# Optimization experiments

Measured on AMD Instinct MI355X. Metric: run time of the kernel, lower is better.

## Reference

```python
import jax, jax.numpy as jnp
import numpy as np

B, NO, NM, NV, E = 16, 512, 128, 64, 256
H, DK, MS, FF = 16, 16, 8, 512
TRANS_MAX = 100.0


def _ln(x):
    m = x.mean(-1, keepdims=True)
    v = ((x - m) ** 2).mean(-1, keepdims=True)
    return (x - m) * jax.lax.rsqrt(v + 1e-5)


def _inv_norm(x):
    # 1 - minmax-normalize over the whole per-batch matrix
    mn = x.min(axis=(1, 2), keepdims=True)
    mx = x.max(axis=(1, 2), keepdims=True)
    return 1.0 - (x - mn) / (mx - mn)


def _adjacency(proc_time, trans_time, MVpair_trans, mask_dyn, mask_ma):
    # masked copy of proc_time
    A_proc = jnp.where(mask_dyn, proc_time, 0.0)
    # keep only the per-row minimum nonzero entry (min_ProcTime_elements)
    nz = jnp.where(A_proc == 0.0, jnp.inf, A_proc)
    mn = nz.min(axis=2, keepdims=True)
    keep = (A_proc == mn) & (A_proc != 0.0)
    A_proc = A_proc * keep.astype(proc_time.dtype)
    A_proc_norm = (A_proc > 0.0).astype(proc_time.dtype)
    # machine-machine masks
    mask2 = mask_ma[:, None, :] & mask_ma[:, :, None]  # [B, nm, nm]
    A_procing = (~mask2).astype(proc_time.dtype)
    A_off = _inv_norm(MVpair_trans)
    tt = jnp.where(mask2, trans_time, TRANS_MAX + 1.0)
    A_on = _inv_norm(tt)
    return A_proc_norm, A_procing, A_off, A_on


def _block(row, col, cost, Wq, Wk, Wv, Wo, mW1, mb1, mW2, mb2, fW1, fb1, fW2, fb2):
    # MatNet-style mixed-score multi-head attention encoding block
    Bb, R, _ = row.shape
    C = col.shape[1]
    q = (row @ Wq).reshape(Bb, R, H, DK).transpose(0, 2, 1, 3)  # bhrd
    k = (col @ Wk).reshape(Bb, C, H, DK).transpose(0, 2, 1, 3)  # bhcd
    v = (col @ Wv).reshape(Bb, C, H, DK).transpose(0, 2, 1, 3)
    dot = jnp.einsum('bhrd,bhcd->bhrc', q, k) / jnp.sqrt(jnp.asarray(DK, row.dtype))
    two = jnp.stack([dot, jnp.broadcast_to(cost[:, None], dot.shape)], axis=-1)  # [B,H,R,C,2]
    hmix = jax.nn.relu(jnp.einsum('bhrct,hts->bhrcs', two, mW1) + mb1[None, :, None, None, :])
    score = jnp.einsum('bhrcs,hso->bhrco', hmix, mW2)[..., 0] + mb2[:, 0][None, :, None, None]
    attn = jax.nn.softmax(score, axis=-1)
    ctx = jnp.einsum('bhrc,bhcd->bhrd', attn, v).transpose(0, 2, 1, 3).reshape(Bb, R, H * DK)
    out1 = _ln(row + ctx @ Wo)
    ffn = jax.nn.relu(out1 @ fW1 + fb1) @ fW2 + fb2
    return _ln(out1 + ffn)


def setup_inputs() -> dict:
    key = jax.random.key(0)
    ks = jax.random.split(key, 24)

    def nrm(i, shape, s=0.05):
        return jax.random.normal(ks[i], shape, jnp.float32) * s

    return {
        'ope_emb': nrm(0, (B, NO, E), 1.0),
        'ma_emb': nrm(1, (B, NM, E), 1.0),
        'veh_emb': nrm(2, (B, NV, E), 1.0),
        'proc_time': jax.random.uniform(ks[3], (B, NO, NM), jnp.float32) * 20.0,
        'offload_trans_time': jax.random.uniform(ks[4], (B, NO, NV), jnp.float32) * TRANS_MAX,
        'trans_time': jax.random.uniform(ks[5], (B, NM, NM), jnp.float32) * TRANS_MAX,
        'MVpair_trans': jax.random.uniform(ks[6], (B, NV, NM), jnp.float32) * TRANS_MAX,
        'mask_dyn_ope_ma_adj': jax.random.bernoulli(ks[7], 0.3, (B, NO, NM)),
        'mask_ma': jax.random.bernoulli(ks[8], 0.7, (B, NM)),
        # stacked params for the 4 blocks: 0=ope, 1=veh, 2=ma1, 3=ma2
        'Wq': nrm(9, (4, E, H * DK)),
        'Wk': nrm(10, (4, E, H * DK)),
        'Wv': nrm(11, (4, E, H * DK)),
        'Wo': nrm(12, (4, H * DK, E)),
        'mixW1': nrm(13, (4, H, 2, MS), 0.3),
        'mixb1': jnp.zeros((4, H, MS), jnp.float32),
        'mixW2': nrm(14, (4, H, MS, 1), 0.3),
        'mixb2': jnp.zeros((4, H, 1), jnp.float32),
        'ffW1': nrm(15, (4, E, FF)),
        'ffb1': jnp.zeros((4, FF), jnp.float32),
        'ffW2': nrm(16, (4, FF, E)),
        'ffb2': jnp.zeros((4, E), jnp.float32),
        'maprojW': nrm(17, (2 * E, E)),
        'maprojb': jnp.zeros((E,), jnp.float32),
    }


def reference(ope_emb, ma_emb, veh_emb, proc_time, offload_trans_time, trans_time,
              MVpair_trans, mask_dyn_ope_ma_adj, mask_ma,
              Wq, Wk, Wv, Wo, mixW1, mixb1, mixW2, mixb2,
              ffW1, ffb1, ffW2, ffb2, maprojW, maprojb):
    A_proc_norm, A_procing, A_off, A_on = _adjacency(
        proc_time, trans_time, MVpair_trans, mask_dyn_ope_ma_adj, mask_ma)

    def blk(i, row, col, cost):
        return _block(row, col, cost, Wq[i], Wk[i], Wv[i], Wo[i],
                      mixW1[i], mixb1[i], mixW2[i], mixb2[i],
                      ffW1[i], ffb1[i], ffW2[i], ffb2[i])

    ope_out = blk(0, ope_emb, ma_emb, A_proc_norm)
    veh_out = blk(1, veh_emb, ma_emb, A_off)
    ma1 = blk(2, ma_emb, ma_emb, A_procing)
    ma2 = blk(3, ma_emb, ma_emb, A_on)
    ma_out = jnp.concatenate([ma1, ma2], axis=-1) @ maprojW + maprojb
    return (ope_out, ma_out, veh_out)
```

## Files before the change

### kernel.cpp

```cpp
#include <hip/hip_runtime.h>
#include <hip/hip_fp16.h>
#include <hip/hip_bf16.h>


typedef unsigned short u16;
typedef __attribute__((ext_vector_type(8))) short bf16x8;
typedef __attribute__((ext_vector_type(4))) float f32x4;
struct us4 { u16 x, y, z, w; };

__device__ __forceinline__ float bf2f(u16 u) {
  return __uint_as_float(((unsigned int)u) << 16);
}
__device__ __forceinline__ u16 f2bf(float f) {
  unsigned int x = __float_as_uint(f);
  x += 0x7FFFu + ((x >> 16) & 1u);
  return (u16)(x >> 16);
}
__device__ __forceinline__ __half2 h2max(__half2 a, __half2 b) {
  unsigned au = *(unsigned*)&a, bu = *(unsigned*)&b, ru;
  asm("v_pk_max_f16 %0, %1, %2" : "=v"(ru) : "v"(au), "v"(bu));
  return *(__half2*)&ru;
}

#define NBATCH 16
#define NOPE   512
#define NMA    128
#define NVEH   64
#define EDIM   256

struct PrepArgs {
  const float* ope; const float* ma; const float* veh;
  u16* ope_bf; u16* ma_bf; u16* veh_bf;
  const float* proc; const int* mask_dyn; float* A_proc;
  const float* mv; const float* trans; const int* mask_ma;
  unsigned int* mm;
};
struct TrArgs {
  const float* Wq; const float* Wk; const float* Wv; const float* Wo;
  const float* ffW1; const float* ffW2; const float* maproj;
  u16* WqT; u16* WkT; u16* WvT; u16* WoT; u16* ffW1T; u16* ffW2T; u16* maprojT;
};
__global__ __launch_bounds__(256) void prep_a(PrepArgs a, TrArgs tr) {
  int blk = blockIdx.x, t = threadIdx.x;
  if (blk < 2816) {
    int i = blk * 256 + t;
    const float* s; u16* d; int j;
    if (i < 524288)      { s = a.ope; d = a.ope_bf; j = i; }
    else if (i < 655360) { s = a.ma;  d = a.ma_bf;  j = i - 524288; }
    else                 { s = a.veh; d = a.veh_bf; j = i - 655360; }
    float4 v = ((const float4*)s)[j];
    us4 o = { f2bf(v.x), f2bf(v.y), f2bf(v.z), f2bf(v.w) };
    ((us4*)d)[j] = o;
    return;
  }
  if (blk < 6912) {
    int local = blk - 2816;
    int row = local * 2 + (t >> 7);
    int lane = t & 127;
    size_t idx = (size_t)row * NMA + lane;
    float av = a.mask_dyn[idx] ? a.proc[idx] : 0.0f;
    float cand = (av != 0.0f) ? av : 1.0e30f;
    __shared__ float red[256];
    red[t] = cand;
    __syncthreads();
    for (int s = 64; s > 0; s >>= 1) {
      if (lane < s) red[t] = fminf(red[t], red[t + s]);
      __syncthreads();
    }
    float mn = red[t & 128];
    a.A_proc[idx] = (av != 0.0f && av == mn) ? 1.0f : 0.0f;
    return;
  }
  if (blk < 7104) {
    __shared__ float smn[256], smx[256];
    float mn = 1.0e30f, mx = -1.0e30f;
    int mmIdx;
    if (blk < 6976) {
      int local = blk - 6912;
      int b = local >> 2, chunk = local & 3;
      const float* xb = a.mv + (size_t)b * 8192 + chunk * 2048;
#pragma unroll
      for (int r = 0; r < 8; r++) {
        float v = xb[r * 256 + t];
        mn = fminf(mn, v);
        mx = fmaxf(mx, v);
      }
      mmIdx = b;
    } else {
      int local = blk - 6976;
      int b = local >> 3, chunk = local & 7;
      __shared__ unsigned char mrow[NMA];
      if (t < NMA) mrow[t] = (unsigned char)(a.mask_ma[(size_t)b * NMA + t] != 0);
      __syncthreads();
      const float* tb = a.trans + (size_t)b * 16384 + chunk * 2048;
      int rbase = chunk * 16;
#pragma unroll
      for (int r = 0; r < 8; r++) {
        int off = r * 256 + t;
        int row = rbase + (off >> 7), col = off & 127;
        bool m2 = mrow[row] && mrow[col];
        float tt = m2 ? tb[off] : 101.0f;
        mn = fminf(mn, tt);
        mx = fmaxf(mx, tt);
      }
      mmIdx = 16 + b;
    }
    smn[t] = mn; smx[t] = mx;
    __syncthreads();
    for (int s = 128; s > 0; s >>= 1) {
      if (t < s) {
        smn[t] = fminf(smn[t], smn[t + s]);
        smx[t] = fmaxf(smx[t], smx[t + s]);
      }
      __syncthreads();
    }
    if (t == 0) {
      atomicMin(&a.mm[mmIdx], __float_as_uint(smn[0]));
      atomicMax(&a.mm[32 + mmIdx], __float_as_uint(smx[0]));
    }
    return;
  }
  {
    int b2 = blk - 7104;
    const float* src; u16* dst; int Kd, Nd, tile;
    if (b2 < 1024) {
      int w = b2 >> 8, i = (b2 >> 6) & 3; tile = b2 & 63;
      const float* sw = (w == 0 ? tr.Wq : w == 1 ? tr.Wk : w == 2 ? tr.Wv : tr.Wo);
      u16* dw = (w == 0 ? tr.WqT : w == 1 ? tr.WkT : w == 2 ? tr.WvT : tr.WoT);
      src = sw + (size_t)i * 65536; dst = dw + (size_t)i * 65536;
      Kd = 256; Nd = 256;
    } else if (b2 < 1536) {
      int z = (b2 - 1024) >> 7; tile = (b2 - 1024) & 127;
      src = tr.ffW1 + (size_t)z * 131072; dst = tr.ffW1T + (size_t)z * 131072;
      Kd = 256; Nd = 512;
    } else {
      int z = (b2 - 1536) >> 7; tile = (b2 - 1536) & 127;
      if (z < 4) { src = tr.ffW2 + (size_t)z * 131072; dst = tr.ffW2T + (size_t)z * 131072; }
      else       { src = tr.maproj; dst = tr.maprojT; }
      Kd = 512; Nd = 256;
    }
    int nx = Nd >> 5;
    int k0 = (tile / nx) * 32, n0 = (tile % nx) * 32;
    __shared__ float tl[32][33];
    int tx = t & 31, ty = t >> 5;
#pragma unroll
    for (int r = 0; r < 4; r++)
      tl[ty + r * 8][tx] = src[(size_t)(k0 + ty + r * 8) * Nd + n0 + tx];
    __syncthreads();
#pragma unroll
    for (int r = 0; r < 4; r++)
      dst[(size_t)(n0 + ty + r * 8) * Kd + k0 + tx] = f2bf(tl[tx][ty + r * 8]);
  }
}

struct PB {
  const float* mv; const float* trans; const int* mask_ma;
  const unsigned int* mm; float* A_offb; float* a_on; float* a_pcing;
};
__device__ __forceinline__ void prep_b_body(const PB& p, int blk, int t) {
  if (blk < 512) {
    int b = blk >> 5, off = (blk & 31) * 256 + t;
    float lo = __uint_as_float(p.mm[b]);
    float inv = 1.0f / (__uint_as_float(p.mm[32 + b]) - lo);
    size_t idx = (size_t)b * 8192 + off;
    p.A_offb[idx] = 1.0f - (p.mv[idx] - lo) * inv;
    return;
  }
  int local = blk - 512;
  int b = local >> 6, off = (local & 63) * 256 + t;
  int row = off >> 7, col = off & 127;
  bool m2 = (p.mask_ma[(size_t)b * NMA + row] != 0) &&
            (p.mask_ma[(size_t)b * NMA + col] != 0);
  size_t idx = (size_t)b * 16384 + off;
  float tt = m2 ? p.trans[idx] : 101.0f;
  float lo = __uint_as_float(p.mm[16 + b]);
  float inv = 1.0f / (__uint_as_float(p.mm[48 + b]) - lo);
  p.a_on[idx] = 1.0f - (tt - lo) * inv;
  p.a_pcing[idx] = m2 ? 0.0f : 1.0f;
}

struct GG {
  const u16* A; const u16* WT; const float* bias; u16* C;
  int M, N, K, epi, wgStart, cshift, mode;
};
struct GGArgs { GG g[12]; PB pb; int n; int nGemmWG; };

__global__ __launch_bounds__(256) void gemm_grouped(GGArgs args) {
  int wg = blockIdx.x;
  if (wg >= args.nGemmWG) {
    prep_b_body(args.pb, wg - args.nGemmWG, threadIdx.x);
    return;
  }
  int gi = 0;
  for (int i = 1; i < args.n; i++)
    if (wg >= args.g[i].wgStart) gi = i;
  GG gg = args.g[gi];
  int lwg = wg - gg.wgStart;
  int bx = lwg & ((1 << gg.cshift) - 1);
  int by = lwg >> gg.cshift;
  int N = gg.N, K = gg.K;

  __shared__ u16 As[128][40];
  __shared__ u16 Bs[128][40];
  int tid = threadIdx.x;
  int lane = tid & 63, wid = tid >> 6;
  int wr = (wid >> 1) * 64, wc = (wid & 1) * 64;
  int m16 = lane & 15, quad = lane >> 4;
  int rb = by * 128, cb = bx * 128;
  int srow = tid >> 2;
  int schunk = (tid & 3) * 8;

  f32x4 acc[4][4];
#pragma unroll
  for (int i = 0; i < 4; i++)
#pragma unroll
    for (int j = 0; j < 4; j++) acc[i][j] = (f32x4){0.f, 0.f, 0.f, 0.f};

  for (int k0 = 0; k0 < K; k0 += 32) {
    uint4 va0 = *(const uint4*)(gg.A + (size_t)(rb + srow) * K + k0 + schunk);
    uint4 va1 = *(const uint4*)(gg.A + (size_t)(rb + 64 + srow) * K + k0 + schunk);
    uint4 vb0 = *(const uint4*)(gg.WT + (size_t)(cb + srow) * K + k0 + schunk);
    uint4 vb1 = *(const uint4*)(gg.WT + (size_t)(cb + 64 + srow) * K + k0 + schunk);
    __syncthreads();
    *(uint4*)&As[srow][schunk] = va0;
    *(uint4*)&As[64 + srow][schunk] = va1;
    *(uint4*)&Bs[srow][schunk] = vb0;
    *(uint4*)&Bs[64 + srow][schunk] = vb1;
    __syncthreads();
    bf16x8 af[4], bfr[4];
#pragma unroll
    for (int i = 0; i < 4; i++)
      af[i] = *(const bf16x8*)&As[wr + i * 16 + m16][quad * 8];
#pragma unroll
    for (int j = 0; j < 4; j++)
      bfr[j] = *(const bf16x8*)&Bs[wc + j * 16 + m16][quad * 8];
#pragma unroll
    for (int i = 0; i < 4; i++)
#pragma unroll
      for (int j = 0; j < 4; j++)
        acc[i][j] = __builtin_amdgcn_mfma_f32_16x16x32_bf16(
            af[i], bfr[j], acc[i][j], 0, 0, 0);
  }

#pragma unroll
  for (int i = 0; i < 4; i++) {
#pragma unroll
    for (int j = 0; j < 4; j++) {
      int col = cb + wc + j * 16 + m16;
      float bv = (gg.epi >= 1) ? gg.bias[col] : 0.0f;
      if (gg.mode == 3) {
        int row0 = rb + wr + i * 16 + quad * 4;
        int b = row0 >> 7, c0 = row0 & 127;
        us4 o = { f2bf(acc[i][j][0]), f2bf(acc[i][j][1]),
                  f2bf(acc[i][j][2]), f2bf(acc[i][j][3]) };
        *(us4*)(gg.C + (size_t)b * 32768 + (size_t)col * 128 + c0) = o;
      } else {
#pragma unroll
        for (int r = 0; r < 4; r++) {
          int row = rb + wr + i * 16 + quad * 4 + r;
          float v = acc[i][j][r] + bv;
          if (gg.epi == 2) v = fmaxf(v, 0.0f);
          size_t off;
          if (gg.mode == 0) {
            off = (size_t)row * N + col;
          } else if (gg.mode == 1) {
            off = ((size_t)(row >> 4)) * 4096 + (size_t)(col >> 4) * 256 +
                  (size_t)(row & 15) * 16 + (col & 15);
          } else {
            off = ((size_t)(row >> 7)) * 32768 + (size_t)(col >> 4) * 2048 +
                  (size_t)(row & 127) * 16 + (col & 15);
          }
          gg.C[off] = f2bf(v);
        }
      }
    }
  }
}

__global__ __launch_bounds__(256) void gemm_mfma_f32(
    const u16* __restrict__ A, const u16* __restrict__ WT,
    const float* __restrict__ bias, float* __restrict__ C,
    int M, int N, int K) {
  __shared__ u16 As[64][40];
  __shared__ u16 Bs[64][40];
  int tid = threadIdx.x;
  int lane = tid & 63, wid = tid >> 6;
  int wr = (wid >> 1) * 32, wc = (wid & 1) * 32;
  int m16 = lane & 15, quad = lane >> 4;
  int rb = blockIdx.y * 64, cb = blockIdx.x * 64;
  int srow = tid >> 2;
  int schunk = (tid & 3) * 8;
  f32x4 acc[2][2];
#pragma unroll
  for (int i = 0; i < 2; i++)
#pragma unroll
    for (int j = 0; j < 2; j++) acc[i][j] = (f32x4){0.f, 0.f, 0.f, 0.f};
  for (int k0 = 0; k0 < K; k0 += 32) {
    uint4 va = *(const uint4*)(A + (size_t)(rb + srow) * K + k0 + schunk);
    uint4 vb = *(const uint4*)(WT + (size_t)(cb + srow) * K + k0 + schunk);
    __syncthreads();
    *(uint4*)&As[srow][schunk] = va;
    *(uint4*)&Bs[srow][schunk] = vb;
    __syncthreads();
    bf16x8 af[2], bfr[2];
#pragma unroll
    for (int i = 0; i < 2; i++)
      af[i] = *(const bf16x8*)&As[wr + i * 16 + m16][quad * 8];
#pragma unroll
    for (int j = 0; j < 2; j++)
      bfr[j] = *(const bf16x8*)&Bs[wc + j * 16 + m16][quad * 8];
#pragma unroll
    for (int i = 0; i < 2; i++)
#pragma unroll
      for (int j = 0; j < 2; j++)
        acc[i][j] = __builtin_amdgcn_mfma_f32_16x16x32_bf16(
            af[i], bfr[j], acc[i][j], 0, 0, 0);
  }
#pragma unroll
  for (int i = 0; i < 2; i++)
#pragma unroll
    for (int j = 0; j < 2; j++) {
      int col = cb + wc + j * 16 + m16;
      float bv = bias[col];
#pragma unroll
      for (int r = 0; r < 4; r++) {
        int row = rb + wr + i * 16 + quad * 4 + r;
        C[(size_t)row * N + col] = acc[i][j][r] + bv;
      }
    }
}

struct AG {
  const u16* q; const u16* k; const u16* vT; const float* cost; u16* ctx;
  const float* w1; const float* b1; const float* w2; const float* b2;
  int R, wgStart;
};
struct AGArgs { AG g[4]; };

#define CSTRIDE 134

__global__ __launch_bounds__(256) void attn_grouped(AGArgs args) {
  int blk = blockIdx.x;
  int gi = 0;
#pragma unroll
  for (int i = 1; i < 4; i++)
    if (blk >= args.g[i].wgStart) gi = i;
  AG gg = args.g[gi];
  int local = blk - gg.wgStart;

  int t = threadIdx.x;
  int wave = t >> 6, lane = t & 63;
  int quad = lane >> 4, l16 = lane & 15;
  int j = local & 15;
  int b = (j & 7) * 2 + (j >> 3);
  int hgrp = (local >> 4) & 1;
  int tile = local >> 5;
  int m0 = b * gg.R + tile * 16;

  __shared__ __half costs_h[16 * CSTRIDE];
  __shared__ u16 pbuf[4][16 * 136];

  const float* cp = gg.cost + (size_t)m0 * 128;
  for (int i = t; i < 2048; i += 256)
    costs_h[(i >> 7) * CSTRIDE + (i & 127)] = __float2half(cp[i]);
  __syncthreads();

  const bf16x8 zerof = (bf16x8){0, 0, 0, 0, 0, 0, 0, 0};
  const f32x4 zacc = (f32x4){0.f, 0.f, 0.f, 0.f};
  const __half2 zh = __float2half2_rn(0.0f);
  u16* pb = pbuf[wave];
  const u16* qtile = gg.q + ((size_t)(m0 >> 4)) * 4096;
  const u16* kb    = gg.k + (size_t)b * 32768;

#pragma unroll
  for (int hh = 0; hh < 2; hh++) {
    int h = hgrp * 8 + wave * 2 + hh;

    __half2 w10h[8], w11h[8], b1h[8], w2h[8];
#pragma unroll
    for (int s = 0; s < 8; s++) {
      w10h[s] = __float2half2_rn(gg.w1[h * 16 + s] * 0.25f);
      w11h[s] = __float2half2_rn(gg.w1[h * 16 + 8 + s]);
      b1h[s]  = __float2half2_rn(gg.b1[h * 8 + s]);
      w2h[s]  = __float2half2_rn(gg.w2[h * 8 + s]);
    }
    float wb2v = gg.b2[h];

    bf16x8 bq = zerof;
    if (quad < 2)
      bq = *(const bf16x8*)(qtile + (size_t)h * 256 + l16 * 16 + quad * 8);
    f32x4 st[8];
    __builtin_amdgcn_s_setprio(1);
#pragma unroll
    for (int ct = 0; ct < 8; ct++) {
      bf16x8 ak = zerof;
      if (quad < 2)
        ak = *(const bf16x8*)(kb + (size_t)h * 2048 + (ct * 16 + l16) * 16 +
                              quad * 8);
      st[ct] = __builtin_amdgcn_mfma_f32_16x16x32_bf16(ak, bq, zacc, 0, 0, 0);
    }
    __builtin_amdgcn_s_setprio(0);

#pragma unroll
    for (int ct = 0; ct < 8; ct++) {
#pragma unroll
      for (int p = 0; p < 2; p++) {
        __half2 d2 = __float22half2_rn(
            make_float2(st[ct][p * 2], st[ct][p * 2 + 1]));
        __half2 c2 = *(const __half2*)&costs_h[l16 * CSTRIDE + ct * 16 +
                                               quad * 4 + p * 2];
        __half2 s2 = zh;
#pragma unroll
        for (int s = 0; s < 8; s++) {
          __half2 hm = __hfma2(d2, w10h[s], __hfma2(c2, w11h[s], b1h[s]));
          hm = h2max(hm, zh);
          s2 = __hfma2(hm, w2h[s], s2);
        }
        float2 sf = __half22float2(s2);
        st[ct][p * 2]     = sf.x + wb2v;
        st[ct][p * 2 + 1] = sf.y + wb2v;
      }
    }

    float mx = -1.0e30f;
#pragma unroll
    for (int ct = 0; ct < 8; ct++)
#pragma unroll
      for (int rg = 0; rg < 4; rg++) mx = fmaxf(mx, st[ct][rg]);
    mx = fmaxf(mx, __shfl_xor(mx, 16, 64));
    mx = fmaxf(mx, __shfl_xor(mx, 32, 64));
    float sum = 0.0f;
#pragma unroll
    for (int ct = 0; ct < 8; ct++)
#pragma unroll
      for (int rg = 0; rg < 4; rg++) {
        float e = __expf(st[ct][rg] - mx);
        st[ct][rg] = e;
        sum += e;
      }
    sum += __shfl_xor(sum, 16, 64);
    sum += __shfl_xor(sum, 32, 64);
    float inv = 1.0f / sum;

#pragma unroll
    for (int ct = 0; ct < 8; ct++) {
#pragma unroll
      for (int p = 0; p < 2; p++) {
        __hip_bfloat162 pk = __float22bfloat162_rn(
            make_float2(st[ct][p * 2] * inv, st[ct][p * 2 + 1] * inv));
        *(unsigned int*)&pb[l16 * 136 + ct * 16 + quad * 4 + p * 2] =
            *(unsigned int*)&pk;
      }
    }

    f32x4 cacc = zacc;
    __builtin_amdgcn_s_setprio(1);
#pragma unroll
    for (int ks = 0; ks < 4; ks++) {
      bf16x8 ap = *(const bf16x8*)&pb[l16 * 136 + ks * 32 + quad * 8];
      bf16x8 bv = *(const bf16x8*)(gg.vT + (size_t)b * 32768 +
                                   (size_t)(h * 16 + l16) * 128 + ks * 32 +
                                   quad * 8);
      cacc = __builtin_amdgcn_mfma_f32_16x16x32_bf16(ap, bv, cacc, 0, 0, 0);
    }
    __builtin_amdgcn_s_setprio(0);

#pragma unroll
    for (int rg = 0; rg < 4; rg++)
      gg.ctx[(size_t)(m0 + quad * 4 + rg) * 256 + h * 16 + l16] =
          f2bf(cacc[rg]);
  }
}

struct FTArgs {
  const u16* ctx;
  const float* rope; const float* rveh; const float* rma;
  const u16* WoT; const u16* W1T; const u16* W2T;
  const float* ffb1; const float* ffb2;
  float* outOpe; float* outVeh; u16* maCat;
};

__global__ __launch_bounds__(256) void fused_tail(FTArgs a) {
  int rb = blockIdx.x * 64;
  int gi = (rb < 8192) ? 0 : (rb < 9216) ? 1 : (rb < 11264) ? 2 : 3;
  const u16* WoT = a.WoT + (size_t)gi * 65536;
  const u16* W1T = a.W1T + (size_t)gi * 131072;
  const u16* W2T = a.W2T + (size_t)gi * 131072;
  const float* b1p = a.ffb1 + gi * 512;
  const float* b2p = a.ffb2 + gi * 256;
  const float* resid; int lr0;
  if (gi == 0)      { resid = a.rope; lr0 = rb; }
  else if (gi == 1) { resid = a.rveh; lr0 = rb - 8192; }
  else if (gi == 2) { resid = a.rma;  lr0 = rb - 9216; }
  else              { resid = a.rma;  lr0 = rb - 11264; }

  __shared__ u16 O1[64][264];
  __shared__ u16 Fs[64][520];
  __shared__ u16 Asg[64][40];
  __shared__ u16 Bsg[256][40];
  __shared__ float redS[64][4];
  __shared__ float redQ[64][4];

  int tid = threadIdx.x;
  int lane = tid & 63, wid = tid >> 6;
  int m16 = lane & 15, quad = lane >> 4;
  int wc = wid * 64;
  int srow = tid >> 2, schunk = (tid & 3) * 8;

  f32x4 acc[4][4];
#pragma unroll
  for (int i = 0; i < 4; i++)
#pragma unroll
    for (int j = 0; j < 4; j++) acc[i][j] = (f32x4){0.f, 0.f, 0.f, 0.f};

  uint4 va = *(const uint4*)(a.ctx + (size_t)(rb + srow) * 256 + schunk);
  uint4 vb[4];
#pragma unroll
  for (int c = 0; c < 4; c++)
    vb[c] = *(const uint4*)(WoT + (size_t)(c * 64 + srow) * 256 + schunk);
  for (int k0 = 0; k0 < 256; k0 += 32) {
    __syncthreads();
    *(uint4*)&Asg[srow][schunk] = va;
#pragma unroll
    for (int c = 0; c < 4; c++)
      *(uint4*)&Bsg[c * 64 + srow][schunk] = vb[c];
    if (k0 + 32 < 256) {
      va = *(const uint4*)(a.ctx + (size_t)(rb + srow) * 256 + k0 + 32 + schunk);
#pragma unroll
      for (int c = 0; c < 4; c++)
        vb[c] = *(const uint4*)(WoT + (size_t)(c * 64 + srow) * 256 + k0 + 32 + schunk);
    }
    __syncthreads();
    bf16x8 af[4], bf[4];
#pragma unroll
    for (int i = 0; i < 4; i++)
      af[i] = *(const bf16x8*)&Asg[i * 16 + m16][quad * 8];
#pragma unroll
    for (int j = 0; j < 4; j++)
      bf[j] = *(const bf16x8*)&Bsg[wc + j * 16 + m16][quad * 8];
#pragma unroll
    for (int i = 0; i < 4; i++)
#pragma unroll
      for (int j = 0; j < 4; j++)
        acc[i][j] = __builtin_amdgcn_mfma_f32_16x16x32_bf16(
            af[i], bf[j], acc[i][j], 0, 0, 0);
  }

#pragma unroll
  for (int i = 0; i < 4; i++)
#pragma unroll
    for (int j = 0; j < 4; j++) {
      int colj = wc + j * 16 + m16;
#pragma unroll
      for (int r = 0; r < 4; r++)
        acc[i][j][r] += resid[(size_t)(lr0 + i * 16 + quad * 4 + r) * 256 + colj];
    }
#pragma unroll
  for (int i = 0; i < 4; i++)
#pragma unroll
    for (int r = 0; r < 4; r++) {
      float s = acc[i][0][r] + acc[i][1][r] + acc[i][2][r] + acc[i][3][r];
      float q = acc[i][0][r] * acc[i][0][r] + acc[i][1][r] * acc[i][1][r] +
                acc[i][2][r] * acc[i][2][r] + acc[i][3][r] * acc[i][3][r];
#pragma unroll
      for (int d = 1; d < 16; d <<= 1) {
        s += __shfl_xor(s, d, 64);
        q += __shfl_xor(q, d, 64);
      }
      if (m16 == 0) {
        redS[i * 16 + quad * 4 + r][wid] = s;
        redQ[i * 16 + quad * 4 + r][wid] = q;
      }
    }
  __syncthreads();
#pragma unroll
  for (int i = 0; i < 4; i++)
#pragma unroll
    for (int r = 0; r < 4; r++) {
      int row = i * 16 + quad * 4 + r;
      float s = redS[row][0] + redS[row][1] + redS[row][2] + redS[row][3];
      float q = redQ[row][0] + redQ[row][1] + redQ[row][2] + redQ[row][3];
      float mean = s * (1.0f / 256.0f);
      float var = q * (1.0f / 256.0f) - mean * mean;
      float rs = rsqrtf(fmaxf(var, 0.0f) + 1e-5f);
#pragma unroll
      for (int j = 0; j < 4; j++)
        O1[row][wc + j * 16 + m16] = f2bf((acc[i][j][r] - mean) * rs);
    }

  for (int p = 0; p < 2; p++) {
#pragma unroll
    for (int i = 0; i < 4; i++)
#pragma unroll
      for (int j = 0; j < 4; j++) acc[i][j] = (f32x4){0.f, 0.f, 0.f, 0.f};
#pragma unroll
    for (int c = 0; c < 4; c++)
      vb[c] = *(const uint4*)(W1T + (size_t)(p * 256 + c * 64 + srow) * 256 + schunk);
    for (int k0 = 0; k0 < 256; k0 += 32) {
      __syncthreads();
#pragma unroll
      for (int c = 0; c < 4; c++)
        *(uint4*)&Bsg[c * 64 + srow][schunk] = vb[c];
      if (k0 + 32 < 256) {
#pragma unroll
        for (int c = 0; c < 4; c++)
          vb[c] = *(const uint4*)(W1T + (size_t)(p * 256 + c * 64 + srow) * 256 +
                                  k0 + 32 + schunk);
      }
      __syncthreads();
      bf16x8 af[4], bf[4];
#pragma unroll
      for (int i = 0; i < 4; i++)
        af[i] = *(const bf16x8*)&O1[i * 16 + m16][k0 + quad * 8];
#pragma unroll
      for (int j = 0; j < 4; j++)
        bf[j] = *(const bf16x8*)&Bsg[wc + j * 16 + m16][quad * 8];
#pragma unroll
      for (int i = 0; i < 4; i++)
#pragma unroll
        for (int j = 0; j < 4; j++)
          acc[i][j] = __builtin_amdgcn_mfma_f32_16x16x32_bf16(
              af[i], bf[j], acc[i][j], 0, 0, 0);
    }
#pragma unroll
    for (int i = 0; i < 4; i++)
#pragma unroll
      for (int j = 0; j < 4; j++) {
        int col = p * 256 + wc + j * 16 + m16;
        float bv = b1p[col];
#pragma unroll
        for (int r = 0; r < 4; r++)
          Fs[i * 16 + quad * 4 + r][col] = f2bf(fmaxf(acc[i][j][r] + bv, 0.0f));
      }
  }

#pragma unroll
  for (int i = 0; i < 4; i++)
#pragma unroll
    for (int j = 0; j < 4; j++) acc[i][j] = (f32x4){0.f, 0.f, 0.f, 0.f};
#pragma unroll
  for (int c = 0; c < 4; c++)
    vb[c] = *(const uint4*)(W2T + (size_t)(c * 64 + srow) * 512 + schunk);
  for (int k0 = 0; k0 < 512; k0 += 32) {
    __syncthreads();
#pragma unroll
    for (int c = 0; c < 4; c++)
      *(uint4*)&Bsg[c * 64 + srow][schunk] = vb[c];
    if (k0 + 32 < 512) {
#pragma unroll
      for (int c = 0; c < 4; c++)
        vb[c] = *(const uint4*)(W2T + (size_t)(c * 64 + srow) * 512 +
                                k0 + 32 + schunk);
    }
    __syncthreads();
    bf16x8 af[4], bf[4];
#pragma unroll
    for (int i = 0; i < 4; i++)
      af[i] = *(const bf16x8*)&Fs[i * 16 + m16][k0 + quad * 8];
#pragma unroll
    for (int j = 0; j < 4; j++)
      bf[j] = *(const bf16x8*)&Bsg[wc + j * 16 + m16][quad * 8];
#pragma unroll
    for (int i = 0; i < 4; i++)
#pragma unroll
      for (int j = 0; j < 4; j++)
        acc[i][j] = __builtin_amdgcn_mfma_f32_16x16x32_bf16(
            af[i], bf[j], acc[i][j], 0, 0, 0);
  }

#pragma unroll
  for (int i = 0; i < 4; i++)
#pragma unroll
    for (int j = 0; j < 4; j++) {
      int colj = wc + j * 16 + m16;
      float bv = b2p[colj];
#pragma unroll
      for (int r = 0; r < 4; r++) {
        int row = i * 16 + quad * 4 + r;
        acc[i][j][r] += bv + bf2f(O1[row][colj]);
      }
    }
#pragma unroll
  for (int i = 0; i < 4; i++)
#pragma unroll
    for (int r = 0; r < 4; r++) {
      float s = acc[i][0][r] + acc[i][1][r] + acc[i][2][r] + acc[i][3][r];
      float q = acc[i][0][r] * acc[i][0][r] + acc[i][1][r] * acc[i][1][r] +
                acc[i][2][r] * acc[i][2][r] + acc[i][3][r] * acc[i][3][r];
#pragma unroll
      for (int d = 1; d < 16; d <<= 1) {
        s += __shfl_xor(s, d, 64);
        q += __shfl_xor(q, d, 64);
      }
      if (m16 == 0) {
        redS[i * 16 + quad * 4 + r][wid] = s;
        redQ[i * 16 + quad * 4 + r][wid] = q;
      }
    }
  __syncthreads();
#pragma unroll
  for (int i = 0; i < 4; i++)
#pragma unroll
    for (int r = 0; r < 4; r++) {
      int row = i * 16 + quad * 4 + r;
      float s = redS[row][0] + redS[row][1] + redS[row][2] + redS[row][3];
      float q = redQ[row][0] + redQ[row][1] + redQ[row][2] + redQ[row][3];
      float mean = s * (1.0f / 256.0f);
      float var = q * (1.0f / 256.0f) - mean * mean;
      float rs = rsqrtf(fmaxf(var, 0.0f) + 1e-5f);
#pragma unroll
      for (int j = 0; j < 4; j++) {
        int colj = wc + j * 16 + m16;
        float y = (acc[i][j][r] - mean) * rs;
        if (gi == 0)
          a.outOpe[(size_t)(lr0 + row) * 256 + colj] = y;
        else if (gi == 1)
          a.outVeh[(size_t)(lr0 + row) * 256 + colj] = y;
        else if (gi == 2)
          a.maCat[(size_t)(lr0 + row) * 512 + colj] = f2bf(y);
        else
          a.maCat[(size_t)(lr0 + row) * 512 + 256 + colj] = f2bf(y);
      }
    }
}

extern "C" void kernel_launch(void* const* d_in, const int* in_sizes, int n_in,
                              void* d_out, int out_size, void* d_ws, size_t ws_size,
                              hipStream_t stream) {
  const float* ope   = (const float*)d_in[0];
  const float* ma    = (const float*)d_in[1];
  const float* veh   = (const float*)d_in[2];
  const float* proc  = (const float*)d_in[3];
  const float* trans = (const float*)d_in[5];
  const float* mv    = (const float*)d_in[6];
  const int* mask_dyn = (const int*)d_in[7];
  const int* mask_ma  = (const int*)d_in[8];
  const float* Wq = (const float*)d_in[9];
  const float* Wk = (const float*)d_in[10];
  const float* Wv = (const float*)d_in[11];
  const float* Wo = (const float*)d_in[12];
  const float* mixW1 = (const float*)d_in[13];
  const float* mixb1 = (const float*)d_in[14];
  const float* mixW2 = (const float*)d_in[15];
  const float* mixb2 = (const float*)d_in[16];
  const float* ffW1 = (const float*)d_in[17];
  const float* ffb1 = (const float*)d_in[18];
  const float* ffW2 = (const float*)d_in[19];
  const float* ffb2 = (const float*)d_in[20];
  const float* maprojW = (const float*)d_in[21];
  const float* maprojb = (const float*)d_in[22];
  float* out = (float*)d_out;
  char* ws = (char*)d_ws;

  const int OFF[4] = {0, 8192, 9216, 11264};
  const int MS4[4] = {8192, 1024, 2048, 2048};

  const size_t MB = 1 << 20;
  float* A_proc  = (float*)(ws + 0);
  float* A_offb  = (float*)(ws + 4 * MB);
  float* A_pcing = (float*)(ws + 4 * MB + MB / 2);
  float* A_on    = (float*)(ws + 5 * MB + MB / 2);
  u16* ope_bf  = (u16*)(ws + 6 * MB + MB / 2);
  u16* ma_bf   = (u16*)(ws + 10 * MB + MB / 2);
  u16* veh_bf  = (u16*)(ws + 11 * MB + MB / 2);
  u16* WqT     = (u16*)(ws + 12 * MB);
  u16* WkT     = (u16*)(ws + 12 * MB + MB / 2);
  u16* WvT     = (u16*)(ws + 13 * MB);
  u16* WoT     = (u16*)(ws + 13 * MB + MB / 2);
  u16* ffW1T   = (u16*)(ws + 14 * MB);
  u16* ffW2T   = (u16*)(ws + 15 * MB);
  u16* maprojT = (u16*)(ws + 16 * MB);
  u16* q_all   = (u16*)(ws + 16 * MB + MB / 2);
  u16* k_all   = (u16*)(ws + 23 * MB);
  u16* vT_all  = (u16*)(ws + 31 * MB);
  u16* ctx_all = (u16*)(ws + 35 * MB);
  u16* maCat   = (u16*)(ws + 67 * MB + MB / 2);
  unsigned int* mmbuf = (unsigned int*)(ws + 70 * MB);

  hipMemsetAsync(mmbuf, 0x7F, 128, stream);
  hipMemsetAsync((char*)mmbuf + 128, 0x00, 128, stream);

  {
    PrepArgs pa = {ope, ma, veh, ope_bf, ma_bf, veh_bf,
                   proc, mask_dyn, A_proc, mv, trans, mask_ma, mmbuf};
    TrArgs ta = {Wq, Wk, Wv, Wo, ffW1, ffW2, maprojW,
                 WqT, WkT, WvT, WoT, ffW1T, ffW2T, maprojT};
    prep_a<<<9280, 256, 0, stream>>>(pa, ta);
  }

  const size_t MA_OUT  = (size_t)NBATCH * NOPE * EDIM;
  const size_t VEH_OUT = MA_OUT + (size_t)NBATCH * NMA * EDIM;

  const u16* rowbf[4] = {ope_bf, veh_bf, ma_bf, ma_bf};
  const float* costp[4] = {A_proc, A_offb, A_pcing, A_on};
  PB pb = {mv, trans, mask_ma, mmbuf, A_offb, A_on, A_pcing};

  {
    GGArgs ga; ga.n = 12; ga.pb = pb;
    int wg = 0;
    for (int i = 0; i < 4; i++) {
      ga.g[i] = {rowbf[i], WqT + (size_t)i * 65536, nullptr,
                 q_all + (size_t)OFF[i] * 256, MS4[i], 256, 256, 0, wg, 1, 1};
      wg += (MS4[i] / 128) * 2;
    }
    for (int i = 0; i < 4; i++) {
      ga.g[4 + i] = {ma_bf, WkT + (size_t)i * 65536, nullptr,
                     k_all + (size_t)i * 524288, 2048, 256, 256, 0, wg, 1, 2};
      wg += 32;
    }
    for (int i = 0; i < 4; i++) {
      ga.g[8 + i] = {ma_bf, WvT + (size_t)i * 65536, nullptr,
                     vT_all + (size_t)i * 524288, 2048, 256, 256, 0, wg, 1, 3};
      wg += 32;
    }
    ga.nGemmWG = wg;
    gemm_grouped<<<wg + 1536, 256, 0, stream>>>(ga);
  }

  {
    AGArgs aa;
    int wg = 0;
    const int R4[4] = {NOPE, NVEH, NMA, NMA};
    for (int i = 0; i < 4; i++) {
      aa.g[i] = {q_all + (size_t)OFF[i] * 256, k_all + (size_t)i * 524288,
                 vT_all + (size_t)i * 524288, costp[i],
                 ctx_all + (size_t)OFF[i] * 256,
                 mixW1 + (size_t)i * 256, mixb1 + (size_t)i * 128,
                 mixW2 + (size_t)i * 128, mixb2 + (size_t)i * 16,
                 R4[i], wg};
      wg += MS4[i] / 8;
    }
    attn_grouped<<<wg, 256, 0, stream>>>(aa);
  }

  {
    FTArgs fa = {ctx_all, ope, veh, ma, WoT, ffW1T, ffW2T, ffb1, ffb2,
                 out, out + VEH_OUT, maCat};
    fused_tail<<<208, 256, 0, stream>>>(fa);
  }

  gemm_mfma_f32<<<dim3(4, 32), 256, 0, stream>>>(maCat, maprojT, maprojb,
      out + MA_OUT, 2048, 256, 512);
}
```

Before: 246.4 us.

## Halve fused_tail row tile, load weights directly from global, interleave FFN halves

```diff
diff --git a/kernel.cpp b/kernel.cpp
--- a/kernel.cpp
+++ b/kernel.cpp
@@ -481,7 +481,7 @@
 };
 
 __global__ __launch_bounds__(256) void fused_tail(FTArgs a) {
-  int rb = blockIdx.x * 64;
+  int rb = blockIdx.x * 32;
   int gi = (rb < 8192) ? 0 : (rb < 9216) ? 1 : (rb < 11264) ? 2 : 3;
   const u16* WoT = a.WoT + (size_t)gi * 65536;
   const u16* W1T = a.W1T + (size_t)gi * 131072;
@@ -494,74 +494,56 @@
   else if (gi == 2) { resid = a.rma;  lr0 = rb - 9216; }
   else              { resid = a.rma;  lr0 = rb - 11264; }
 
-  __shared__ u16 O1[64][264];
-  __shared__ u16 Fs[64][520];
-  __shared__ u16 Asg[64][40];
-  __shared__ u16 Bsg[256][40];
-  __shared__ float redS[64][4];
-  __shared__ float redQ[64][4];
+  __shared__ u16 O1[32][264];
+  __shared__ u16 Fs[32][264];
+  __shared__ float redS[32][4];
+  __shared__ float redQ[32][4];
 
   int tid = threadIdx.x;
   int lane = tid & 63, wid = tid >> 6;
   int m16 = lane & 15, quad = lane >> 4;
   int wc = wid * 64;
-  int srow = tid >> 2, schunk = (tid & 3) * 8;
-
-  f32x4 acc[4][4];
-#pragma unroll
-  for (int i = 0; i < 4; i++)
-#pragma unroll
-    for (int j = 0; j < 4; j++) acc[i][j] = (f32x4){0.f, 0.f, 0.f, 0.f};
-
-  uint4 va = *(const uint4*)(a.ctx + (size_t)(rb + srow) * 256 + schunk);
-  uint4 vb[4];
-#pragma unroll
-  for (int c = 0; c < 4; c++)
-    vb[c] = *(const uint4*)(WoT + (size_t)(c * 64 + srow) * 256 + schunk);
+
+  f32x4 acc1[2][4];
+#pragma unroll
+  for (int i = 0; i < 2; i++)
+#pragma unroll
+    for (int j = 0; j < 4; j++) acc1[i][j] = (f32x4){0.f, 0.f, 0.f, 0.f};
+#pragma unroll
   for (int k0 = 0; k0 < 256; k0 += 32) {
-    __syncthreads();
-    *(uint4*)&Asg[srow][schunk] = va;
-#pragma unroll
-    for (int c = 0; c < 4; c++)
-      *(uint4*)&Bsg[c * 64 + srow][schunk] = vb[c];
-    if (k0 + 32 < 256) {
-      va = *(const uint4*)(a.ctx + (size_t)(rb + srow) * 256 + k0 + 32 + schunk);
-#pragma unroll
-      for (int c = 0; c < 4; c++)
-        vb[c] = *(const uint4*)(WoT + (size_t)(c * 64 + srow) * 256 + k0 + 32 + schunk);
-    }
-    __syncthreads();
-    bf16x8 af[4], bf[4];
-#pragma unroll
-    for (int i = 0; i < 4; i++)
-      af[i] = *(const bf16x8*)&Asg[i * 16 + m16][quad * 8];
+    bf16x8 af[2], bf[4];
+#pragma unroll
+    for (int i = 0; i < 2; i++)
+      af[i] = *(const bf16x8*)(a.ctx + (size_t)(rb + i * 16 + m16) * 256 +
+                               k0 + quad * 8);
 #pragma unroll
     for (int j = 0; j < 4; j++)
-      bf[j] = *(const bf16x8*)&Bsg[wc + j * 16 + m16][quad * 8];
-#pragma unroll
-    for (int i = 0; i < 4; i++)
+      bf[j] = *(const bf16x8*)(WoT + (size_t)(wc + j * 16 + m16) * 256 +
+                               k0 + quad * 8);
+#pragma unroll
+    for (int i = 0; i < 2; i++)
 #pragma unroll
       for (int j = 0; j < 4; j++)
-        acc[i][j] = __builtin_amdgcn_mfma_f32_16x16x32_bf16(
-            af[i], bf[j], acc[i][j], 0, 0, 0);
-  }
-
-#pragma unroll
-  for (int i = 0; i < 4; i++)
+        acc1[i][j] = __builtin_amdgcn_mfma_f32_16x16x32_bf16(
+            af[i], bf[j], acc1[i][j], 0, 0, 0);
+  }
+
+#pragma unroll
+  for (int i = 0; i < 2; i++)
 #pragma unroll
     for (int j = 0; j < 4; j++) {
       int colj = wc + j * 16 + m16;
 #pragma unroll
       for (int r = 0; r < 4; r++)
-        acc[i][j][r] += resid[(size_t)(lr0 + i * 16 + quad * 4 + r) * 256 + colj];
-    }
-#pragma unroll
-  for (int i = 0; i < 4; i++)
+        acc1[i][j][r] += resid[(size_t)(lr0 + i * 16 + quad * 4 + r) * 256 + colj];
+    }
+#pragma unroll
+  for (int i = 0; i < 2; i++)
 #pragma unroll
     for (int r = 0; r < 4; r++) {
-      float s = acc[i][0][r] + acc[i][1][r] + acc[i][2][r] + acc[i][3][r];
-      float q = acc[i][0][r] * acc[i][0][r] + acc[i][1][r] * acc[i][1][r] +
-                acc[i][2][r] * acc[i][2][r] + acc[i][3][r] * acc[i][3][r];
+      float s = acc1[i][0][r] + acc1[i][1][r] + acc1[i][2][r] + acc1[i][3][r];
+      float q = acc1[i][0][r] * acc1[i][0][r] + acc1[i][1][r] * acc1[i][1][r] +
+                acc1[i][2][r] * acc1[i][2][r] + acc1[i][3][r] * acc1[i][3][r];
 #pragma unroll
       for (int d = 1; d < 16; d <<= 1) {
         s += __shfl_xor(s, d, 64);
@@ -574,7 +556,7 @@
     }
   __syncthreads();
 #pragma unroll
-  for (int i = 0; i < 4; i++)
+  for (int i = 0; i < 2; i++)
 #pragma unroll
     for (int r = 0; r < 4; r++) {
       int row = i * 16 + quad * 4 + r;
@@ -585,91 +567,73 @@
       float rs = rsqrtf(fmaxf(var, 0.0f) + 1e-5f);
 #pragma unroll
       for (int j = 0; j < 4; j++)
-        O1[row][wc + j * 16 + m16] = f2bf((acc[i][j][r] - mean) * rs);
-    }
-
-  for (int p = 0; p < 2; p++) {
-#pragma unroll
-    for (int i = 0; i < 4; i++)
-#pragma unroll
-      for (int j = 0; j < 4; j++) acc[i][j] = (f32x4){0.f, 0.f, 0.f, 0.f};
-#pragma unroll
-    for (int c = 0; c < 4; c++)
-      vb[c] = *(const uint4*)(W1T + (size_t)(p * 256 + c * 64 + srow) * 256 + schunk);
+        O1[row][wc + j * 16 + m16] = f2bf((acc1[i][j][r] - mean) * rs);
+    }
+  __syncthreads();
+
+  f32x4 acc3[2][4];
+#pragma unroll
+  for (int i = 0; i < 2; i++)
+#pragma unroll
+    for (int j = 0; j < 4; j++) acc3[i][j] = (f32x4){0.f, 0.f, 0.f, 0.f};
+
+  for (int h = 0; h < 2; h++) {
+    const u16* W1h = W1T + (size_t)h * 256 * 256;
+    f32x4 acc2[2][4];
+#pragma unroll
+    for (int i = 0; i < 2; i++)
+#pragma unroll
+      for (int j = 0; j < 4; j++) acc2[i][j] = (f32x4){0.f, 0.f, 0.f, 0.f};
+#pragma unroll
     for (int k0 = 0; k0 < 256; k0 += 32) {
-      __syncthreads();
-#pragma unroll
-      for (int c = 0; c < 4; c++)
-        *(uint4*)&Bsg[c * 64 + srow][schunk] = vb[c];
-      if (k0 + 32 < 256) {
-#pragma unroll
-        for (int c = 0; c < 4; c++)
-          vb[c] = *(const uint4*)(W1T + (size_t)(p * 256 + c * 64 + srow) * 256 +
-                                  k0 + 32 + schunk);
-      }
-      __syncthreads();
-      bf16x8 af[4], bf[4];
-#pragma unroll
-      for (int i = 0; i < 4; i++)
+      bf16x8 af[2], bf[4];
+#pragma unroll
+      for (int i = 0; i < 2; i++)
         af[i] = *(const bf16x8*)&O1[i * 16 + m16][k0 + quad * 8];
 #pragma unroll
       for (int j = 0; j < 4; j++)
-        bf[j] = *(const bf16x8*)&Bsg[wc + j * 16 + m16][quad * 8];
-#pragma unroll
-      for (int i = 0; i < 4; i++)
+        bf[j] = *(const bf16x8*)(W1h + (size_t)(wc + j * 16 + m16) * 256 +
+                                 k0 + quad * 8);
+#pragma unroll
+      for (int i = 0; i < 2; i++)
 #pragma unroll
         for (int j = 0; j < 4; j++)
-          acc[i][j] = __builtin_amdgcn_mfma_f32_16x16x32_bf16(
-              af[i], bf[j], acc[i][j], 0, 0, 0);
-    }
-#pragma unroll
-    for (int i = 0; i < 4; i++)
+          acc2[i][j] = __builtin_amdgcn_mfma_f32_16x16x32_bf16(
+              af[i], bf[j], acc2[i][j], 0, 0, 0);
+    }
+#pragma unroll
+    for (int i = 0; i < 2; i++)
 #pragma unroll
       for (int j = 0; j < 4; j++) {
-        int col = p * 256 + wc + j * 16 + m16;
-        float bv = b1p[col];
+        int coll = wc + j * 16 + m16;
+        float bv = b1p[h * 256 + coll];
 #pragma unroll
         for (int r = 0; r < 4; r++)
-          Fs[i * 16 + quad * 4 + r][col] = f2bf(fmaxf(acc[i][j][r] + bv, 0.0f));
-      }
-  }
-
-#pragma unroll
-  for (int i = 0; i < 4; i++)
-#pragma unroll
-    for (int j = 0; j < 4; j++) acc[i][j] = (f32x4){0.f, 0.f, 0.f, 0.f};
-#pragma unroll
-  for (int c = 0; c < 4; c++)
-    vb[c] = *(const uint4*)(W2T + (size_t)(c * 64 + srow) * 512 + schunk);
-  for (int k0 = 0; k0 < 512; k0 += 32) {
+          Fs[i * 16 + quad * 4 + r][coll] = f2bf(fmaxf(acc2[i][j][r] + bv, 0.0f));
+      }
     __syncthreads();
 #pragma unroll
-    for (int c = 0; c < 4; c++)
-      *(uint4*)&Bsg[c * 64 + srow][schunk] = vb[c];
-    if (k0 + 32 < 512) {
-#pragma unroll
-      for (int c = 0; c < 4; c++)
-        vb[c] = *(const uint4*)(W2T + (size_t)(c * 64 + srow) * 512 +
-                                k0 + 32 + schunk);
+    for (int k0 = 0; k0 < 256; k0 += 32) {
+      bf16x8 af[2], bf[4];
+#pragma unroll
+      for (int i = 0; i < 2; i++)
+        af[i] = *(const bf16x8*)&Fs[i * 16 + m16][k0 + quad * 8];
+#pragma unroll
+      for (int j = 0; j < 4; j++)
+        bf[j] = *(const bf16x8*)(W2T + (size_t)(wc + j * 16 + m16) * 512 +
+                                 h * 256 + k0 + quad * 8);
+#pragma unroll
+      for (int i = 0; i < 2; i++)
+#pragma unroll
+        for (int j = 0; j < 4; j++)
+          acc3[i][j] = __builtin_amdgcn_mfma_f32_16x16x32_bf16(
+              af[i], bf[j], acc3[i][j], 0, 0, 0);
     }
     __syncthreads();
-    bf16x8 af[4], bf[4];
-#pragma unroll
-    for (int i = 0; i < 4; i++)
-      af[i] = *(const bf16x8*)&Fs[i * 16 + m16][k0 + quad * 8];
-#pragma unroll
-    for (int j = 0; j < 4; j++)
-      bf[j] = *(const bf16x8*)&Bsg[wc + j * 16 + m16][quad * 8];
-#pragma unroll
-    for (int i = 0; i < 4; i++)
-#pragma unroll
-      for (int j = 0; j < 4; j++)
-        acc[i][j] = __builtin_amdgcn_mfma_f32_16x16x32_bf16(
-            af[i], bf[j], acc[i][j], 0, 0, 0);
-  }
-
-#pragma unroll
-  for (int i = 0; i < 4; i++)
+  }
+
+#pragma unroll
+  for (int i = 0; i < 2; i++)
 #pragma unroll
     for (int j = 0; j < 4; j++) {
       int colj = wc + j * 16 + m16;
@@ -677,16 +641,16 @@
 #pragma unroll
       for (int r = 0; r < 4; r++) {
         int row = i * 16 + quad * 4 + r;
-        acc[i][j][r] += bv + bf2f(O1[row][colj]);
-      }
-    }
-#pragma unroll
-  for (int i = 0; i < 4; i++)
+        acc3[i][j][r] += bv + bf2f(O1[row][colj]);
+      }
+    }
+#pragma unroll
+  for (int i = 0; i < 2; i++)
 #pragma unroll
     for (int r = 0; r < 4; r++) {
-      float s = acc[i][0][r] + acc[i][1][r] + acc[i][2][r] + acc[i][3][r];
-      float q = acc[i][0][r] * acc[i][0][r] + acc[i][1][r] * acc[i][1][r] +
-                acc[i][2][r] * acc[i][2][r] + acc[i][3][r] * acc[i][3][r];
+      float s = acc3[i][0][r] + acc3[i][1][r] + acc3[i][2][r] + acc3[i][3][r];
+      float q = acc3[i][0][r] * acc3[i][0][r] + acc3[i][1][r] * acc3[i][1][r] +
+                acc3[i][2][r] * acc3[i][2][r] + acc3[i][3][r] * acc3[i][3][r];
 #pragma unroll
       for (int d = 1; d < 16; d <<= 1) {
         s += __shfl_xor(s, d, 64);
@@ -699,7 +663,7 @@
     }
   __syncthreads();
 #pragma unroll
-  for (int i = 0; i < 4; i++)
+  for (int i = 0; i < 2; i++)
 #pragma unroll
     for (int r = 0; r < 4; r++) {
       int row = i * 16 + quad * 4 + r;
@@ -711,7 +675,7 @@
 #pragma unroll
       for (int j = 0; j < 4; j++) {
         int colj = wc + j * 16 + m16;
-        float y = (acc[i][j][r] - mean) * rs;
+        float y = (acc3[i][j][r] - mean) * rs;
         if (gi == 0)
           a.outOpe[(size_t)(lr0 + row) * 256 + colj] = y;
         else if (gi == 1)
@@ -836,7 +800,7 @@
   {
     FTArgs fa = {ctx_all, ope, veh, ma, WoT, ffW1T, ffW2T, ffb1, ffb2,
                  out, out + VEH_OUT, maCat};
-    fused_tail<<<208, 256, 0, stream>>>(fa);
+    fused_tail<<<416, 256, 0, stream>>>(fa);
   }
 
   gemm_mfma_f32<<<dim3(4, 32), 256, 0, stream>>>(maCat, maprojT, maprojb,
```

After: 233.9 us, median of 2. 1.05x faster.
